# Performance work log

Hardware: AMD Instinct MI355X
Metric: run time of the kernel (lower is better)

## Reference

```python
import jax, jax.numpy as jnp
import numpy as np

NUM_GRAPHS = 64
NEG_SLOPE = 0.1


def gcn_conv(x, src, dst, W, b, num_nodes):
    h = x @ W  # [N, out]
    ones = jnp.ones(src.shape[0], dtype=x.dtype)
    deg = jax.ops.segment_sum(ones, dst, num_segments=num_nodes) + 1.0  # +1 self-loop
    dinv = jax.lax.rsqrt(deg)  # deg >= 1 always
    coef = dinv[src] * dinv[dst]  # [E]
    agg = jax.ops.segment_sum(h[src] * coef[:, None], dst, num_segments=num_nodes)
    # self-loop contribution: dinv[i]^2 * h[i]
    out = agg + h * (dinv * dinv)[:, None] + b
    return out


def leaky_relu(x):
    return jnp.where(x >= 0, x, NEG_SLOPE * x)


def global_mean_pool(x, batch, num_graphs):
    s = jax.ops.segment_sum(x, batch, num_segments=num_graphs)
    cnt = jax.ops.segment_sum(jnp.ones(x.shape[0], dtype=x.dtype), batch, num_segments=num_graphs)
    return s / jnp.maximum(cnt, 1.0)[:, None]


def setup_inputs() -> dict:
    key = jax.random.key(0)
    ks = jax.random.split(key, 10)
    N, E, D_IN, D_H, D_OUT, C = 50000, 600000, 128, 128, 128, 16
    x = jax.random.normal(ks[0], (N, D_IN), dtype=jnp.float32)
    edge_index = jax.random.randint(ks[1], (2, E), 0, N, dtype=jnp.int32)
    batch = jnp.sort(jax.random.randint(ks[2], (N,), 0, NUM_GRAPHS, dtype=jnp.int32))
    def glorot(k, shape):
        lim = np.sqrt(6.0 / (shape[0] + shape[1]))
        return jax.random.uniform(k, shape, jnp.float32, -lim, lim)
    W1 = glorot(ks[3], (D_IN, D_H))
    b1 = jnp.zeros((D_H,), jnp.float32)
    W2 = glorot(ks[4], (D_H, D_OUT))
    b2 = jnp.zeros((D_OUT,), jnp.float32)
    Wl = glorot(ks[5], (D_OUT, C))
    bl = jnp.zeros((C,), jnp.float32)
    return {"x": x, "edge_index": edge_index, "batch": batch,
            "W1": W1, "b1": b1, "W2": W2, "b2": b2, "Wl": Wl, "bl": bl}


def reference(x, edge_index, batch, W1, b1, W2, b2, Wl, bl):
    N = x.shape[0]
    src, dst = edge_index[0], edge_index[1]
    h = gcn_conv(x, src, dst, W1, b1, N)
    h = leaky_relu(h)
    h = gcn_conv(h, src, dst, W2, b2, N)
    h = leaky_relu(h)
    g = global_mean_pool(h, batch, NUM_GRAPHS)  # [G, D_OUT]
    # dropout p=0.2 is identity in eval mode
    return g @ Wl + bl
```

## Files before the change

### kernel.cpp

```cpp
#include <hip/hip_runtime.h>

#define D 128
#define NG 64
#define NC 16
#define NEG 0.1f

typedef __attribute__((ext_vector_type(8))) short bf16x8;
typedef __attribute__((ext_vector_type(4))) float f32x4;

__device__ __forceinline__ float bf2f(unsigned int u16) {
    union { unsigned int i; float f; } c;
    c.i = u16 << 16;
    return c.f;
}
__device__ __forceinline__ unsigned short f2bf(float f) {
    union { float f; unsigned int i; } c;
    c.f = f;
    unsigned int i = c.i;
    unsigned int r = (i + 0x7FFFu + ((i >> 16) & 1u)) >> 16;
    return (unsigned short)r;
}

__global__ __launch_bounds__(256) void prep_gemm1_kernel(
        const float* __restrict__ x, const float* __restrict__ W1,
        unsigned int* __restrict__ C, int gb,
        const float* __restrict__ W2, unsigned short* __restrict__ Wf2,
        float* __restrict__ pooled,
        const int* __restrict__ dst, int* __restrict__ deg, int E, int N) {
    __shared__ uint4 Ws[2048];
    int b = blockIdx.x;
    int tid = threadIdx.x;
    if (b < gb) {
        int w = tid >> 6, lane = tid & 63;
        int quad = lane >> 4, m16 = lane & 15;
        int rowstart = b * 64;
#pragma unroll
        for (int i = 0; i < 8; i++) {
            int fid = tid + 256 * i;
            int fm = fid & 15;
            int fquad = (fid >> 4) & 3;
            int fkc = (fid >> 6) & 3;
            int ft = fid >> 8;
            int n = ft * 16 + fm;
            int k0 = fkc * 32 + fquad * 8;
            unsigned short r[8];
#pragma unroll
            for (int j = 0; j < 8; j++) r[j] = f2bf(W1[(k0 + j) * 128 + n]);
            uint4 v;
            v.x = (unsigned int)r[0] | ((unsigned int)r[1] << 16);
            v.y = (unsigned int)r[2] | ((unsigned int)r[3] << 16);
            v.z = (unsigned int)r[4] | ((unsigned int)r[5] << 16);
            v.w = (unsigned int)r[6] | ((unsigned int)r[7] << 16);
            Ws[fid] = v;
        }

        int arow = rowstart + 16 * w + m16;
        bool valid = arow < N;
        bf16x8 af[4];
#pragma unroll
        for (int kc = 0; kc < 4; kc++) {
            float4 f0 = make_float4(0.f, 0.f, 0.f, 0.f), f1 = f0;
            if (valid) {
                const float4* p = (const float4*)(x + (size_t)arow * 128 + kc * 32 + quad * 8);
                f0 = p[0];
                f1 = p[1];
            }
            bf16x8 a;
            a[0] = (short)f2bf(f0.x); a[1] = (short)f2bf(f0.y);
            a[2] = (short)f2bf(f0.z); a[3] = (short)f2bf(f0.w);
            a[4] = (short)f2bf(f1.x); a[5] = (short)f2bf(f1.y);
            a[6] = (short)f2bf(f1.z); a[7] = (short)f2bf(f1.w);
            af[kc] = a;
        }
        __syncthreads();

        f32x4 acc[8];
#pragma unroll
        for (int t = 0; t < 8; t++) acc[t] = (f32x4){0.f, 0.f, 0.f, 0.f};
#pragma unroll
        for (int t = 0; t < 8; t++) {
#pragma unroll
            for (int kc = 0; kc < 4; kc++) {
                bf16x8 bh = *(const bf16x8*)&Ws[(((t * 4 + kc) * 4 + quad) * 16 + m16)];
                acc[t] = __builtin_amdgcn_mfma_f32_16x16x32_bf16(af[kc], bh, acc[t], 0, 0, 0);
            }
        }
#pragma unroll
        for (int t = 0; t < 8; t++) {
#pragma unroll
            for (int r = 0; r < 4; r++) {
                int row = rowstart + 16 * w + quad * 4 + r;
                unsigned int us = f2bf(acc[t][r]);
                unsigned int other = (unsigned int)__shfl_xor((int)us, 1);
                if (((m16 & 1) == 0) && row < N)
                    C[(size_t)row * 64 + t * 8 + (m16 >> 1)] = us | (other << 16);
            }
        }
    } else {
        int bb = b - gb;
        if (bb < 8) {
            int fid = bb * 256 + tid;
            int m = fid & 15;
            int quad = (fid >> 4) & 3;
            int kc = (fid >> 6) & 3;
            int t = fid >> 8;
            int n = t * 16 + m;
            int k0 = kc * 32 + quad * 8;
            unsigned short r[8];
#pragma unroll
            for (int j = 0; j < 8; j++) r[j] = f2bf(W2[(k0 + j) * 128 + n]);
            uint4 v;
            v.x = (unsigned int)r[0] | ((unsigned int)r[1] << 16);
            v.y = (unsigned int)r[2] | ((unsigned int)r[3] << 16);
            v.z = (unsigned int)r[4] | ((unsigned int)r[5] << 16);
            v.w = (unsigned int)r[6] | ((unsigned int)r[7] << 16);
            ((uint4*)Wf2)[fid] = v;
        } else if (bb < 40) {
            pooled[(bb - 8) * 256 + tid] = 0.f;
        } else {
            int e = (bb - 40) * 256 + tid;
            if (e < E) atomicAdd(&deg[dst[e]], 1);
        }
    }
}

__global__ void scan_block_kernel(const int* __restrict__ deg, int* __restrict__ scan1,
                                  int* __restrict__ blocksum, float* __restrict__ dinv, int N) {
    __shared__ int sm[256];
    int tid = threadIdx.x;
    int i = blockIdx.x * 256 + tid;
    int v = (i < N) ? deg[i] : 0;
    if (i < N) dinv[i] = 1.0f / sqrtf((float)v + 1.0f);
    sm[tid] = v;
    __syncthreads();
    for (int off = 1; off < 256; off <<= 1) {
        int t = (tid >= off) ? sm[tid - off] : 0;
        __syncthreads();
        sm[tid] += t;
        __syncthreads();
    }
    if (i < N) scan1[i] = sm[tid];
    if (tid == 255) blocksum[blockIdx.x] = sm[255];
}

__global__ void finalize_ptr_kernel(const int* __restrict__ deg, const int* __restrict__ scan1,
                                    const int* __restrict__ blocksum, int* __restrict__ ptr,
                                    int* __restrict__ fill, int nb, int N, int E) {
    __shared__ int sm[256];
    int tid = threadIdx.x;
    int v = (tid < nb) ? blocksum[tid] : 0;
    sm[tid] = v;
    __syncthreads();
    for (int off = 1; off < 256; off <<= 1) {
        int t = (tid >= off) ? sm[tid - off] : 0;
        __syncthreads();
        sm[tid] += t;
        __syncthreads();
    }
    int blockoff = (blockIdx.x > 0) ? sm[blockIdx.x - 1] : 0;
    int i = blockIdx.x * 256 + tid;
    if (i < N) {
        int p = scan1[i] - deg[i] + blockoff;
        ptr[i] = p;
        fill[i] = p;
        if (i == N - 1) ptr[N] = E;
    }
}

__global__ void scatter_kernel(const int* __restrict__ src, const int* __restrict__ dst,
                               int* __restrict__ fill, const float* __restrict__ dinv,
                               int2* __restrict__ csr_edge, int E) {
    int e = blockIdx.x * blockDim.x + threadIdx.x;
    if (e < E) {
        int d = dst[e];
        int s = src[e];
        int pos = atomicAdd(&fill[d], 1);
        float coef = dinv[s] * dinv[d];
        csr_edge[pos] = make_int2(s, __float_as_int(coef));
    }
}

__global__ __launch_bounds__(256) void gemm_mfma_kernel(const unsigned short* __restrict__ Ag,
                                                        const uint4* __restrict__ Wf,
                                                        unsigned int* __restrict__ C, int N) {
    __shared__ uint4 Ws[2048];
    int tid = threadIdx.x;
    int w = tid >> 6, lane = tid & 63;
    int quad = lane >> 4, m = lane & 15;
    int rowstart = blockIdx.x * 64;

#pragma unroll
    for (int i = 0; i < 8; i++) Ws[tid + 256 * i] = Wf[tid + 256 * i];

    int arow = rowstart + 16 * w + m;
    bool valid = arow < N;
    bf16x8 af[4];
#pragma unroll
    for (int kc = 0; kc < 4; kc++) {
        bf16x8 a;
#pragma unroll
        for (int j = 0; j < 8; j++) a[j] = 0;
        if (valid) a = *(const bf16x8*)(Ag + (size_t)arow * 128 + kc * 32 + quad * 8);
        af[kc] = a;
    }
    __syncthreads();

    f32x4 acc[8];
#pragma unroll
    for (int t = 0; t < 8; t++) acc[t] = (f32x4){0.f, 0.f, 0.f, 0.f};

#pragma unroll
    for (int t = 0; t < 8; t++) {
#pragma unroll
        for (int kc = 0; kc < 4; kc++) {
            bf16x8 bh = *(const bf16x8*)&Ws[(((t * 4 + kc) * 4 + quad) * 16 + m)];
            acc[t] = __builtin_amdgcn_mfma_f32_16x16x32_bf16(af[kc], bh, acc[t], 0, 0, 0);
        }
    }

#pragma unroll
    for (int t = 0; t < 8; t++) {
#pragma unroll
        for (int r = 0; r < 4; r++) {
            int row = rowstart + 16 * w + quad * 4 + r;
            unsigned int us = f2bf(acc[t][r]);
            unsigned int other = (unsigned int)__shfl_xor((int)us, 1);
            if (((m & 1) == 0) && row < N)
                C[(size_t)row * 64 + t * 8 + (m >> 1)] = us | (other << 16);
        }
    }
}

#define ACC8(v, c)                                                         \
    a0 += bf2f((v).x & 0xffffu) * (c); a1 += bf2f((v).x >> 16) * (c);      \
    a2 += bf2f((v).y & 0xffffu) * (c); a3 += bf2f((v).y >> 16) * (c);      \
    a4 += bf2f((v).z & 0xffffu) * (c); a5 += bf2f((v).z >> 16) * (c);      \
    a6 += bf2f((v).w & 0xffffu) * (c); a7 += bf2f((v).w >> 16) * (c);

__global__ __launch_bounds__(256) void combine_kernel(const uint4* __restrict__ h4,
                                                      const int* __restrict__ ptr,
                                                      const int2* __restrict__ csr_edge,
                                                      const float* __restrict__ dinv,
                                                      const float* __restrict__ b,
                                                      uint4* __restrict__ out4, int N) {
    __shared__ int2 smeta[4][64];
    int wave = threadIdx.x >> 6;
    int lane = threadIdx.x & 63;
    int q = lane >> 4;
    int l16 = lane & 15;
    int nb = blockIdx.x * 16 + wave * 4;
    if (nb >= N) return;
    int node = nb + q;
    bool valid = node < N;

    int wlo = ptr[nb];
    int whi = ptr[min(nb + 4, N)];
    int lo = valid ? ptr[node] : 0;
    int hi = valid ? ptr[node + 1] : 0;

    float di = valid ? dinv[node] : 0.f;
    uint4 sv = valid ? h4[(size_t)node * 16 + l16] : make_uint4(0u, 0u, 0u, 0u);
    float4 bv0 = ((const float4*)b)[l16 * 2];
    float4 bv1 = ((const float4*)b)[l16 * 2 + 1];

    float a0 = 0.f, a1 = 0.f, a2 = 0.f, a3 = 0.f, a4 = 0.f, a5 = 0.f, a6 = 0.f, a7 = 0.f;

#pragma unroll 1
    for (int base = wlo; base < whi; base += 64) {
        if (base + lane < whi) smeta[wave][lane] = csr_edge[base + lane];
        int s = max(lo, base);
        int e = min(hi, base + 64);
        int j = s;
#pragma unroll 1
        for (; j + 3 < e; j += 4) {
            int k = j - base;
            int2 e0 = smeta[wave][k];
            int2 e1 = smeta[wave][k + 1];
            int2 e2 = smeta[wave][k + 2];
            int2 e3 = smeta[wave][k + 3];
            uint4 v0 = h4[(size_t)e0.x * 16 + l16];
            uint4 v1 = h4[(size_t)e1.x * 16 + l16];
            uint4 v2 = h4[(size_t)e2.x * 16 + l16];
            uint4 v3 = h4[(size_t)e3.x * 16 + l16];
            float c0 = __int_as_float(e0.y);
            float c1 = __int_as_float(e1.y);
            float c2 = __int_as_float(e2.y);
            float c3 = __int_as_float(e3.y);
            ACC8(v0, c0)
            ACC8(v1, c1)
            ACC8(v2, c2)
            ACC8(v3, c3)
        }
#pragma unroll 1
        for (; j < e; j++) {
            int k = j - base;
            int2 e0 = smeta[wave][k];
            uint4 v0 = h4[(size_t)e0.x * 16 + l16];
            float c0 = __int_as_float(e0.y);
            ACC8(v0, c0)
        }
    }

    if (!valid) return;
    float dd = di * di;
    float v0 = a0 + bf2f(sv.x & 0xffffu) * dd + bv0.x;
    float v1 = a1 + bf2f(sv.x >> 16) * dd + bv0.y;
    float v2 = a2 + bf2f(sv.y & 0xffffu) * dd + bv0.z;
    float v3 = a3 + bf2f(sv.y >> 16) * dd + bv0.w;
    float v4 = a4 + bf2f(sv.z & 0xffffu) * dd + bv1.x;
    float v5 = a5 + bf2f(sv.z >> 16) * dd + bv1.y;
    float v6 = a6 + bf2f(sv.w & 0xffffu) * dd + bv1.z;
    float v7 = a7 + bf2f(sv.w >> 16) * dd + bv1.w;
    v0 = (v0 >= 0.f) ? v0 : NEG * v0;
    v1 = (v1 >= 0.f) ? v1 : NEG * v1;
    v2 = (v2 >= 0.f) ? v2 : NEG * v2;
    v3 = (v3 >= 0.f) ? v3 : NEG * v3;
    v4 = (v4 >= 0.f) ? v4 : NEG * v4;
    v5 = (v5 >= 0.f) ? v5 : NEG * v5;
    v6 = (v6 >= 0.f) ? v6 : NEG * v6;
    v7 = (v7 >= 0.f) ? v7 : NEG * v7;
    uint4 pv;
    pv.x = (unsigned int)f2bf(v0) | ((unsigned int)f2bf(v1) << 16);
    pv.y = (unsigned int)f2bf(v2) | ((unsigned int)f2bf(v3) << 16);
    pv.z = (unsigned int)f2bf(v4) | ((unsigned int)f2bf(v5) << 16);
    pv.w = (unsigned int)f2bf(v6) | ((unsigned int)f2bf(v7) << 16);
    out4[(size_t)node * 16 + l16] = pv;
}

#define PROWS 128
__global__ void pool_accum_kernel(const unsigned int* __restrict__ a2,
                                  const int* __restrict__ batch,
                                  float* __restrict__ pooled, int N) {
    int wave = threadIdx.x >> 6;
    int lane = threadIdx.x & 63;
    int start = blockIdx.x * PROWS;
    int end = start + PROWS;
    if (end > N) end = N;
    float s0 = 0.f, s1 = 0.f;
    int curg = -1;
    for (int r = start + wave; r < end; r += 4) {
        int g = batch[r];
        if (g != curg) {
            if (curg >= 0) {
                atomicAdd(&pooled[curg * D + 2 * lane], s0);
                atomicAdd(&pooled[curg * D + 2 * lane + 1], s1);
            }
            curg = g;
            s0 = 0.f;
            s1 = 0.f;
        }
        unsigned int v = a2[(size_t)r * 64 + lane];
        s0 += bf2f(v & 0xffffu);
        s1 += bf2f(v >> 16);
    }
    if (curg >= 0) {
        atomicAdd(&pooled[curg * D + 2 * lane], s0);
        atomicAdd(&pooled[curg * D + 2 * lane + 1], s1);
    }
}

__global__ void final_kernel(const float* __restrict__ pooled, const int* __restrict__ batch,
                             const float* __restrict__ Wl, const float* __restrict__ bl,
                             float* __restrict__ out, int N) {
    int t = blockIdx.x * blockDim.x + threadIdx.x;
    if (t >= NG * NC) return;
    int g = t >> 4, c = t & 15;
    int l = 0, h = N;
    while (l < h) { int m = (l + h) >> 1; if (batch[m] < g) l = m + 1; else h = m; }
    int lo = l;
    h = N;
    while (l < h) { int m = (l + h) >> 1; if (batch[m] < g + 1) l = m + 1; else h = m; }
    int cnt = l - lo;
    float inv = 1.0f / (float)(cnt > 0 ? cnt : 1);
    float dot = 0.f;
    for (int k = 0; k < D; k++) dot += pooled[g * D + k] * Wl[k * NC + c];
    out[t] = dot * inv + bl[c];
}

extern "C" void kernel_launch(void* const* d_in, const int* in_sizes, int n_in,
                              void* d_out, int out_size, void* d_ws, size_t ws_size,
                              hipStream_t stream) {
    const float* x = (const float*)d_in[0];
    const int* ei = (const int*)d_in[1];
    const int* batch = (const int*)d_in[2];
    const float* W1 = (const float*)d_in[3];
    const float* b1 = (const float*)d_in[4];
    const float* W2 = (const float*)d_in[5];
    const float* b2 = (const float*)d_in[6];
    const float* Wlin = (const float*)d_in[7];
    const float* bl = (const float*)d_in[8];
    float* out = (float*)d_out;

    int N = in_sizes[0] / D;
    int E = in_sizes[1] / 2;
    const int* src = ei;
    const int* dst = ei + E;

    float* ws = (float*)d_ws;
    size_t o = 0;
    unsigned int* bufA = (unsigned int*)(ws + o); o += (size_t)N * 64;
    unsigned int* bufB = (unsigned int*)(ws + o); o += (size_t)N * 64;
    int* deg = (int*)(ws + o);      o += N;
    int* fill = (int*)(ws + o);     o += N;
    float* dinv = ws + o;           o += N;
    int* scan1 = (int*)(ws + o);    o += N;
    int* blocksum = (int*)(ws + o); o += 256;
    int* csr_ptr = (int*)(ws + o);  o += (N + 4);
    int2* csr_edge = (int2*)(ws + o); o += (size_t)2 * E;
    float* pooled = ws + o;         o += NG * D;
    unsigned short* Wf2 = (unsigned short*)(ws + o); o += 8192;

    hipMemsetAsync(deg, 0, (size_t)N * sizeof(int), stream);

    int tb = 256;
    int nscan = (N + 255) / 256;
    int gblocks = (N + 63) / 64;
    int cblocks = (N + 15) / 16;
    int eblocks = (E + 255) / 256;

    prep_gemm1_kernel<<<gblocks + 40 + eblocks, 256, 0, stream>>>(
        x, W1, (unsigned int*)bufA, gblocks, W2, Wf2, pooled, dst, deg, E, N);
    scan_block_kernel<<<nscan, 256, 0, stream>>>(deg, scan1, blocksum, dinv, N);
    finalize_ptr_kernel<<<nscan, 256, 0, stream>>>(deg, scan1, blocksum, csr_ptr, fill,
                                                   nscan, N, E);
    scatter_kernel<<<(E + tb - 1) / tb, tb, 0, stream>>>(src, dst, fill, dinv,
                                                         csr_edge, E);

    combine_kernel<<<cblocks, 256, 0, stream>>>((const uint4*)bufA, csr_ptr, csr_edge,
                                                dinv, b1, (uint4*)bufB, N);
    gemm_mfma_kernel<<<gblocks, 256, 0, stream>>>((const unsigned short*)bufB,
                                                  (const uint4*)Wf2,
                                                  (unsigned int*)bufA, N);
    combine_kernel<<<cblocks, 256, 0, stream>>>((const uint4*)bufA, csr_ptr, csr_edge,
                                                dinv, b2, (uint4*)bufB, N);
    pool_accum_kernel<<<(N + PROWS - 1) / PROWS, 256, 0, stream>>>(bufB, batch, pooled, N);
    final_kernel<<<(NG * NC + tb - 1) / tb, tb, 0, stream>>>(pooled, batch, Wlin, bl, out, N);
}
```

Before: 236.4 us.

## Fuse first GCN aggregation with second-layer GEMM in one kernel

The first-layer combine kernel and the separate MFMA GEMM kernel are merged. Each block aggregates 16 nodes, applies bias and leaky ReLU, stages the bf16 rows in shared memory, and multiplies them by W2 with MFMA. This removes the round trip of the intermediate activations through global memory and one kernel launch. In exchange, W2 is read from global or L2 by every block instead of being staged once per 64 rows in LDS, and the GEMM phase waits on the slowest wave's aggregation.

```diff
diff --git a/kernel.cpp b/kernel.cpp
--- a/kernel.cpp
+++ b/kernel.cpp
@@ -180,62 +180,128 @@
     }
 }
 
-__global__ __launch_bounds__(256) void gemm_mfma_kernel(const unsigned short* __restrict__ Ag,
-                                                        const uint4* __restrict__ Wf,
-                                                        unsigned int* __restrict__ C, int N) {
-    __shared__ uint4 Ws[2048];
-    int tid = threadIdx.x;
-    int w = tid >> 6, lane = tid & 63;
-    int quad = lane >> 4, m = lane & 15;
-    int rowstart = blockIdx.x * 64;
-
-#pragma unroll
-    for (int i = 0; i < 8; i++) Ws[tid + 256 * i] = Wf[tid + 256 * i];
-
-    int arow = rowstart + 16 * w + m;
-    bool valid = arow < N;
-    bf16x8 af[4];
-#pragma unroll
-    for (int kc = 0; kc < 4; kc++) {
-        bf16x8 a;
-#pragma unroll
-        for (int j = 0; j < 8; j++) a[j] = 0;
-        if (valid) a = *(const bf16x8*)(Ag + (size_t)arow * 128 + kc * 32 + quad * 8);
-        af[kc] = a;
-    }
-    __syncthreads();
-
-    f32x4 acc[8];
-#pragma unroll
-    for (int t = 0; t < 8; t++) acc[t] = (f32x4){0.f, 0.f, 0.f, 0.f};
-
-#pragma unroll
-    for (int t = 0; t < 8; t++) {
-#pragma unroll
-        for (int kc = 0; kc < 4; kc++) {
-            bf16x8 bh = *(const bf16x8*)&Ws[(((t * 4 + kc) * 4 + quad) * 16 + m)];
-            acc[t] = __builtin_amdgcn_mfma_f32_16x16x32_bf16(af[kc], bh, acc[t], 0, 0, 0);
-        }
-    }
-
-#pragma unroll
-    for (int t = 0; t < 8; t++) {
-#pragma unroll
-        for (int r = 0; r < 4; r++) {
-            int row = rowstart + 16 * w + quad * 4 + r;
-            unsigned int us = f2bf(acc[t][r]);
-            unsigned int other = (unsigned int)__shfl_xor((int)us, 1);
-            if (((m & 1) == 0) && row < N)
-                C[(size_t)row * 64 + t * 8 + (m >> 1)] = us | (other << 16);
-        }
-    }
-}
-
 #define ACC8(v, c)                                                         \
     a0 += bf2f((v).x & 0xffffu) * (c); a1 += bf2f((v).x >> 16) * (c);      \
     a2 += bf2f((v).y & 0xffffu) * (c); a3 += bf2f((v).y >> 16) * (c);      \
     a4 += bf2f((v).z & 0xffffu) * (c); a5 += bf2f((v).z >> 16) * (c);      \
     a6 += bf2f((v).w & 0xffffu) * (c); a7 += bf2f((v).w >> 16) * (c);
+
+__global__ __launch_bounds__(256) void combine_gemm_kernel(
+        const uint4* __restrict__ h4,
+        const int* __restrict__ ptr,
+        const int2* __restrict__ csr_edge,
+        const float* __restrict__ dinv,
+        const float* __restrict__ b,
+        const uint4* __restrict__ Wf2,
+        unsigned int* __restrict__ C,
+        int N) {
+    __shared__ int2 smeta[4][64];
+    __shared__ unsigned int rowt[16 * 68];
+    int wave = threadIdx.x >> 6;
+    int lane = threadIdx.x & 63;
+    int q = lane >> 4;
+    int l16 = lane & 15;
+    int bb = blockIdx.x * 16;
+    int nb = bb + wave * 4;
+    int node = nb + q;
+    bool valid = node < N;
+
+    if (nb < N) {
+        int wlo = ptr[nb];
+        int whi = ptr[min(nb + 4, N)];
+        int lo = valid ? ptr[node] : 0;
+        int hi = valid ? ptr[node + 1] : 0;
+
+        float di = valid ? dinv[node] : 0.f;
+        uint4 sv = valid ? h4[(size_t)node * 16 + l16] : make_uint4(0u, 0u, 0u, 0u);
+        float4 bv0 = ((const float4*)b)[l16 * 2];
+        float4 bv1 = ((const float4*)b)[l16 * 2 + 1];
+
+        float a0 = 0.f, a1 = 0.f, a2 = 0.f, a3 = 0.f, a4 = 0.f, a5 = 0.f, a6 = 0.f, a7 = 0.f;
+
+#pragma unroll 1
+        for (int base = wlo; base < whi; base += 64) {
+            if (base + lane < whi) smeta[wave][lane] = csr_edge[base + lane];
+            int s = max(lo, base);
+            int e = min(hi, base + 64);
+            int j = s;
+#pragma unroll 1
+            for (; j + 3 < e; j += 4) {
+                int k = j - base;
+                int2 e0 = smeta[wave][k];
+                int2 e1 = smeta[wave][k + 1];
+                int2 e2 = smeta[wave][k + 2];
+                int2 e3 = smeta[wave][k + 3];
+                uint4 v0 = h4[(size_t)e0.x * 16 + l16];
+                uint4 v1 = h4[(size_t)e1.x * 16 + l16];
+                uint4 v2 = h4[(size_t)e2.x * 16 + l16];
+                uint4 v3 = h4[(size_t)e3.x * 16 + l16];
+                float c0 = __int_as_float(e0.y);
+                float c1 = __int_as_float(e1.y);
+                float c2 = __int_as_float(e2.y);
+                float c3 = __int_as_float(e3.y);
+                ACC8(v0, c0)
+                ACC8(v1, c1)
+                ACC8(v2, c2)
+                ACC8(v3, c3)
+            }
+#pragma unroll 1
+            for (; j < e; j++) {
+                int k = j - base;
+                int2 e0 = smeta[wave][k];
+                uint4 v0 = h4[(size_t)e0.x * 16 + l16];
+                float c0 = __int_as_float(e0.y);
+                ACC8(v0, c0)
+            }
+        }
+
+        if (valid) {
+            float dd = di * di;
+            float v0 = a0 + bf2f(sv.x & 0xffffu) * dd + bv0.x;
+            float v1 = a1 + bf2f(sv.x >> 16) * dd + bv0.y;
+            float v2 = a2 + bf2f(sv.y & 0xffffu) * dd + bv0.z;
+            float v3 = a3 + bf2f(sv.y >> 16) * dd + bv0.w;
+            float v4 = a4 + bf2f(sv.z & 0xffffu) * dd + bv1.x;
+            float v5 = a5 + bf2f(sv.z >> 16) * dd + bv1.y;
+            float v6 = a6 + bf2f(sv.w & 0xffffu) * dd + bv1.z;
+            float v7 = a7 + bf2f(sv.w >> 16) * dd + bv1.w;
+            v0 = (v0 >= 0.f) ? v0 : NEG * v0;
+            v1 = (v1 >= 0.f) ? v1 : NEG * v1;
+            v2 = (v2 >= 0.f) ? v2 : NEG * v2;
+            v3 = (v3 >= 0.f) ? v3 : NEG * v3;
+            v4 = (v4 >= 0.f) ? v4 : NEG * v4;
+            v5 = (v5 >= 0.f) ? v5 : NEG * v5;
+            v6 = (v6 >= 0.f) ? v6 : NEG * v6;
+            v7 = (v7 >= 0.f) ? v7 : NEG * v7;
+            unsigned int* p = &rowt[(wave * 4 + q) * 68 + l16 * 4];
+            p[0] = (unsigned int)f2bf(v0) | ((unsigned int)f2bf(v1) << 16);
+            p[1] = (unsigned int)f2bf(v2) | ((unsigned int)f2bf(v3) << 16);
+            p[2] = (unsigned int)f2bf(v4) | ((unsigned int)f2bf(v5) << 16);
+            p[3] = (unsigned int)f2bf(v6) | ((unsigned int)f2bf(v7) << 16);
+        }
+    }
+    __syncthreads();
+
+#pragma unroll
+    for (int tt = 0; tt < 2; tt++) {
+        int t = wave * 2 + tt;
+        f32x4 acc = (f32x4){0.f, 0.f, 0.f, 0.f};
+#pragma unroll
+        for (int kc = 0; kc < 4; kc++) {
+            bf16x8 a = *(const bf16x8*)&rowt[l16 * 68 + kc * 16 + q * 4];
+            bf16x8 bh = *(const bf16x8*)&Wf2[((t * 4 + kc) * 4 + q) * 16 + l16];
+            acc = __builtin_amdgcn_mfma_f32_16x16x32_bf16(a, bh, acc, 0, 0, 0);
+        }
+#pragma unroll
+        for (int r = 0; r < 4; r++) {
+            int row = bb + q * 4 + r;
+            unsigned int us = f2bf(acc[r]);
+            unsigned int other = (unsigned int)__shfl_xor((int)us, 1);
+            if (((l16 & 1) == 0) && row < N)
+                C[(size_t)row * 64 + t * 8 + (l16 >> 1)] = us | (other << 16);
+        }
+    }
+}
 
 __global__ __launch_bounds__(256) void combine_kernel(const uint4* __restrict__ h4,
                                                       const int* __restrict__ ptr,
@@ -426,13 +492,11 @@
     scatter_kernel<<<(E + tb - 1) / tb, tb, 0, stream>>>(src, dst, fill, dinv,
                                                          csr_edge, E);
 
-    combine_kernel<<<cblocks, 256, 0, stream>>>((const uint4*)bufA, csr_ptr, csr_edge,
-                                                dinv, b1, (uint4*)bufB, N);
-    gemm_mfma_kernel<<<gblocks, 256, 0, stream>>>((const unsigned short*)bufB,
-                                                  (const uint4*)Wf2,
-                                                  (unsigned int*)bufA, N);
-    combine_kernel<<<cblocks, 256, 0, stream>>>((const uint4*)bufA, csr_ptr, csr_edge,
-                                                dinv, b2, (uint4*)bufB, N);
-    pool_accum_kernel<<<(N + PROWS - 1) / PROWS, 256, 0, stream>>>(bufB, batch, pooled, N);
+    combine_gemm_kernel<<<cblocks, 256, 0, stream>>>((const uint4*)bufA, csr_ptr, csr_edge,
+                                                     dinv, b1, (const uint4*)Wf2,
+                                                     (unsigned int*)bufB, N);
+    combine_kernel<<<cblocks, 256, 0, stream>>>((const uint4*)bufB, csr_ptr, csr_edge,
+                                                dinv, b2, (uint4*)bufA, N);
+    pool_accum_kernel<<<(N + PROWS - 1) / PROWS, 256, 0, stream>>>(bufA, batch, pooled, N);
     final_kernel<<<(NG * NC + tb - 1) / tb, tb, 0, stream>>>(pooled, batch, Wlin, bl, out, N);
 }
```

After: 227.3 us. 1.04x faster.
